# Kernel tuning notes

Measured on AMD Instinct MI355X. Metric: run time of the kernel, lower is better.

## Reference

```python
import jax, jax.numpy as jnp
import numpy as np
from jax import lax

NBITS = 8
QMAX_SYM = 2 ** (NBITS - 1) - 1  # 127
QMIN_SYM = -(2 ** (NBITS - 1))   # -128
QMAX_ASYM = 2 ** NBITS - 1       # 255


def fake_quant_sym(x):
    # symmetric per-tensor fake quant with straight-through estimator
    delta = lax.stop_gradient(jnp.max(jnp.abs(x))) / QMAX_SYM + 1e-8
    q = jnp.clip(jnp.round(x / delta), QMIN_SYM, QMAX_SYM) * delta
    return x + lax.stop_gradient(q - x)


def fake_quant_asym(x):
    # asymmetric per-tensor fake quant (for softmax output) with STE
    xmin = lax.stop_gradient(jnp.min(x))
    xmax = lax.stop_gradient(jnp.max(x))
    delta = (xmax - xmin) / QMAX_ASYM + 1e-8
    zp = jnp.round(-xmin / delta)
    q = (jnp.clip(jnp.round(x / delta) + zp, 0, QMAX_ASYM) - zp) * delta
    return x + lax.stop_gradient(q - x)


def layer_norm(x, g, b, eps=1e-5):
    mu = jnp.mean(x, axis=-1, keepdims=True)
    var = jnp.var(x, axis=-1, keepdims=True)
    return (x - mu) * lax.rsqrt(var + eps) * g + b


def setup_inputs() -> dict:
    key = jax.random.key(0)
    ks = jax.random.split(key, 8)
    B, N, C = 8, 4096, 256
    s = 0.02
    return {
        "x": jax.random.normal(ks[0], (B, N, C), jnp.float32),
        "q_w": jax.random.normal(ks[1], (C, C), jnp.float32) * s,
        "q_b": jnp.zeros((C,), jnp.float32),
        "kv_w": jax.random.normal(ks[2], (2 * C, C), jnp.float32) * s,
        "kv_b": jnp.zeros((2 * C,), jnp.float32),
        "sr_w": jax.random.normal(ks[3], (C, C, 4, 4), jnp.float32) * s,
        "sr_b": jnp.zeros((C,), jnp.float32),
        "norm_g": jnp.ones((C,), jnp.float32),
        "norm_b": jnp.zeros((C,), jnp.float32),
        "proj_w": jax.random.normal(ks[4], (C, C), jnp.float32) * s,
        "proj_b": jnp.zeros((C,), jnp.float32),
        "H": 64,
        "W": 64,
    }


def reference(x, q_w, q_b, kv_w, kv_b, sr_w, sr_b, norm_g, norm_b, proj_w, proj_b, H, W):
    B, N, C = x.shape
    num_heads = 8
    sr_ratio = 4
    dh = C // num_heads
    scale = dh ** -0.5

    # weight fake-quant (PreQuantModule, sym=True)
    q_wq = fake_quant_sym(q_w)
    kv_wq = fake_quant_sym(kv_w)
    sr_wq = fake_quant_sym(sr_w)
    proj_wq = fake_quant_sym(proj_w)

    # q projection -> [B, heads, N, dh], post-act sym fake quant
    q = (jnp.einsum('bnc,dc->bnd', x, q_wq) + q_b)
    q = fake_quant_sym(q.reshape(B, N, num_heads, dh).transpose(0, 2, 1, 3))

    # spatial reduction: x -> [B,C,H,W], conv k=stride=sr_ratio, then LayerNorm
    x_ = x.transpose(0, 2, 1).reshape(B, C, H, W)
    x_ = lax.conv_general_dilated(x_, sr_wq, (sr_ratio, sr_ratio), 'VALID',
                                  dimension_numbers=('NCHW', 'OIHW', 'NCHW'))
    x_ = x_ + sr_b[None, :, None, None]
    N2 = (H // sr_ratio) * (W // sr_ratio)
    x_ = x_.reshape(B, C, N2).transpose(0, 2, 1)  # [B, N2, C]
    x_ = layer_norm(x_, norm_g, norm_b)

    # kv projection -> k, v [B, heads, N2, dh], post-act sym fake quant
    kv = jnp.einsum('bnc,dc->bnd', x_, kv_wq) + kv_b
    kv = kv.reshape(B, N2, 2, num_heads, dh).transpose(2, 0, 3, 1, 4)
    k = fake_quant_sym(kv[0])
    v = fake_quant_sym(kv[1])

    # attention with asym fake quant on softmax output
    attn = jnp.einsum('bhnd,bhmd->bhnm', q, k) * scale
    attn = jax.nn.softmax(attn, axis=-1)
    attn = fake_quant_asym(attn)

    out = jnp.einsum('bhnm,bhmd->bhnd', attn, v)
    out = out.transpose(0, 2, 1, 3).reshape(B, N, C)
    out = jnp.einsum('bnc,dc->bnd', out, proj_wq) + proj_b
    return out
```

## Files before the change

### kernel.cpp

```cpp
#include <hip/hip_runtime.h>
#include <stdint.h>

typedef float f32x4 __attribute__((ext_vector_type(4)));
typedef __bf16 bf16x8 __attribute__((ext_vector_type(8)));

#define DEV __device__ __forceinline__

DEV unsigned short f2bf(float f) {
  unsigned u = __float_as_uint(f);
  u += 0x7FFFu + ((u >> 16) & 1u);
  return (unsigned short)(u >> 16);
}

DEV float exp2_(float x) {
#if __has_builtin(__builtin_amdgcn_exp2f)
  return __builtin_amdgcn_exp2f(x);
#else
  return exp2f(x);
#endif
}

DEV unsigned cvtpk(float lo, float hi) {
  unsigned r;
  asm("v_cvt_pk_bf16_f32 %0, %1, %2" : "=v"(r) : "v"(lo), "v"(hi));
  return r;
}

DEV void pl32swap(unsigned &a, unsigned &b) {
#if __has_builtin(__builtin_amdgcn_permlane32_swap)
  auto r = __builtin_amdgcn_permlane32_swap(a, b, false, false);
  a = r[0]; b = r[1];
#else
  asm("v_permlane32_swap_b32 %0, %1" : "+v"(a), "+v"(b));
#endif
}

DEV void pl16swap(unsigned &a, unsigned &b) {
#if __has_builtin(__builtin_amdgcn_permlane16_swap)
  auto r = __builtin_amdgcn_permlane16_swap(a, b, false, false);
  a = r[0]; b = r[1];
#else
  asm("v_permlane16_swap_b32 %0, %1" : "+v"(a), "+v"(b));
#endif
}

DEV uint4 qfrag4(uint4 w, float idq, float dq) {
  unsigned o[4];
  const unsigned* wi = &w.x;
  #pragma unroll
  for (int i = 0; i < 4; i++) {
    float lo = __uint_as_float(wi[i] << 16);
    float hi = __uint_as_float(wi[i] & 0xffff0000u);
    lo = fminf(fmaxf(rintf(lo * idq), -128.f), 127.f) * dq;
    hi = fminf(fmaxf(rintf(hi * idq), -128.f), 127.f) * dq;
    o[i] = cvtpk(lo, hi);
  }
  return make_uint4(o[0], o[1], o[2], o[3]);
}

DEV bf16x8 qfrag(uint4 w, float idq, float dq) {
  uint4 r = qfrag4(w, idq, dq);
  return *(bf16x8*)&r;
}

__global__ void k_init(float* scal) {
  int t = threadIdx.x;
  if (t < 16) scal[t] = (t == 7) ? __uint_as_float(0x7f800000u) : 0.f;
}

__global__ __launch_bounds__(256) void k_absmax4(const float* w0, const float* w1,
                                                 const float* w2, const float* w3, float* scal) {
  const float* srcs[4] = {w0, w1, w2, w3};
  const int ns[4] = {65536, 131072, 1048576, 65536};
  int t = blockIdx.y;
  const float* src = srcs[t];
  int n = ns[t];
  float m = 0.f;
  for (int i = blockIdx.x * 256 + threadIdx.x; i < n; i += gridDim.x * 256)
    m = fmaxf(m, fabsf(src[i]));
  #pragma unroll
  for (int d = 1; d < 64; d <<= 1) m = fmaxf(m, __shfl_xor(m, d, 64));
  __shared__ float red[4];
  if ((threadIdx.x & 63) == 0) red[threadIdx.x >> 6] = m;
  __syncthreads();
  if (threadIdx.x == 0) {
    m = fmaxf(fmaxf(red[0], red[1]), fmaxf(red[2], red[3]));
    atomicMax((unsigned*)(scal + t), __float_as_uint(m));
  }
}

__global__ __launch_bounds__(256) void k_quantw(const float* qw, const float* kvw,
                                                const float* prw, const float* srw,
                                                const float* xf,
                                                unsigned short* qo, unsigned short* kvo,
                                                unsigned short* pro, unsigned short* sro,
                                                unsigned short* xbo,
                                                const float* scal) {
  int bx = blockIdx.x;
  int tid = bx * 256 + threadIdx.x;
  {
    int oo = tid >> 12;
    int rem = tid & 4095;
    int khkw = rem >> 8;
    int i = rem & 255;
    float delta = scal[2] / 127.f + 1e-8f;
    float x = srw[oo * 4096 + i * 16 + khkw];
    sro[tid] = f2bf(fminf(fmaxf(rintf(x / delta), -128.f), 127.f) * delta);
  }
  {
    const float4* xs = (const float4*)(xf + (size_t)tid * 8);
    float4 v0 = xs[0], v1 = xs[1];
    unsigned w0 = ((unsigned)f2bf(v0.y) << 16) | f2bf(v0.x);
    unsigned w1 = ((unsigned)f2bf(v0.w) << 16) | f2bf(v0.z);
    unsigned w2 = ((unsigned)f2bf(v1.y) << 16) | f2bf(v1.x);
    unsigned w3 = ((unsigned)f2bf(v1.w) << 16) | f2bf(v1.z);
    *(uint4*)(xbo + (size_t)tid * 8) = make_uint4(w0, w1, w2, w3);
  }
  if (bx < 512) {
    float delta = scal[1] / 127.f + 1e-8f;
    kvo[tid] = f2bf(fminf(fmaxf(rintf(kvw[tid] / delta), -128.f), 127.f) * delta);
  }
  if (bx < 256) {
    float dq = scal[0] / 127.f + 1e-8f;
    qo[tid] = f2bf(fminf(fmaxf(rintf(qw[tid] / dq), -128.f), 127.f) * dq);
    float dp = scal[3] / 127.f + 1e-8f;
    pro[tid] = f2bf(fminf(fmaxf(rintf(prw[tid] / dp), -128.f), 127.f) * dp);
  }
}

__global__ __launch_bounds__(256) void k_gemm_qkv(const unsigned short* __restrict__ xnrm,
                                                  const unsigned short* __restrict__ kvw,
                                                  const float* __restrict__ kvb,
                                                  const unsigned short* __restrict__ xb,
                                                  const unsigned short* __restrict__ qw,
                                                  const float* __restrict__ qb,
                                                  unsigned short* __restrict__ kqu,
                                                  unsigned short* __restrict__ vqtu,
                                                  unsigned short* __restrict__ qq,
                                                  float* scal) {
  __shared__ unsigned short smem[18432];
  const int tid = threadIdx.x;
  const int wid = tid >> 6, lane = tid & 63;
  const int quad = lane >> 4, lr = lane & 15;
  const int wm = wid >> 1, wn = wid & 1;
  if (blockIdx.x < 256) {
    unsigned short* As = smem;
    unsigned short* Bs = smem + 8704;
    const int n0 = (blockIdx.x & 7) * 64, m0 = (blockIdx.x >> 3) * 64;
    f32x4 acc[2][2] = {};
    for (int kb = 0; kb < 256; kb += 128) {
      __syncthreads();
      #pragma unroll
      for (int i = 0; i < 4; i++) {
        int c = i * 256 + tid;
        int row = c >> 4, cu = (c & 15) * 8;
        *(uint4*)&As[row * 136 + cu] = *(const uint4*)(xnrm + (size_t)(m0 + row) * 256 + kb + cu);
        *(uint4*)&Bs[row * 136 + cu] = *(const uint4*)(kvw + (size_t)(n0 + row) * 256 + kb + cu);
      }
      __syncthreads();
      #pragma unroll
      for (int kc = 0; kc < 4; kc++) {
        bf16x8 af0 = *(const bf16x8*)&As[(wm * 32 + lr) * 136 + kc * 32 + quad * 8];
        bf16x8 af1 = *(const bf16x8*)&As[(wm * 32 + 16 + lr) * 136 + kc * 32 + quad * 8];
        bf16x8 bf0 = *(const bf16x8*)&Bs[(wn * 32 + lr) * 136 + kc * 32 + quad * 8];
        bf16x8 bf1 = *(const bf16x8*)&Bs[(wn * 32 + 16 + lr) * 136 + kc * 32 + quad * 8];
        acc[0][0] = __builtin_amdgcn_mfma_f32_16x16x32_bf16(af0, bf0, acc[0][0], 0, 0, 0);
        acc[0][1] = __builtin_amdgcn_mfma_f32_16x16x32_bf16(af0, bf1, acc[0][1], 0, 0, 0);
        acc[1][0] = __builtin_amdgcn_mfma_f32_16x16x32_bf16(af1, bf0, acc[1][0], 0, 0, 0);
        acc[1][1] = __builtin_amdgcn_mfma_f32_16x16x32_bf16(af1, bf1, acc[1][1], 0, 0, 0);
      }
    }
    float amax = 0.f;
    #pragma unroll
    for (int mi = 0; mi < 2; mi++)
      #pragma unroll
      for (int ni = 0; ni < 2; ni++) {
        int col = n0 + wn * 32 + ni * 16 + lr;
        float bv = kvb[col];
        #pragma unroll
        for (int r = 0; r < 4; r++) {
          int row = m0 + wm * 32 + mi * 16 + quad * 4 + r;
          float v = acc[mi][ni][r] + bv;
          int b = row >> 8, n2 = row & 255;
          int h = (col >> 5) & 7, j = col & 31;
          if (col < 256)
            kqu[((size_t)((b * 8 + h) * 256 + n2)) * 32 + j] = f2bf(v);
          else
            vqtu[((size_t)((b * 8 + h) * 32 + j)) * 256 + n2] = f2bf(v);
          amax = fmaxf(amax, fabsf(v));
        }
      }
    #pragma unroll
    for (int d = 1; d < 64; d <<= 1) amax = fmaxf(amax, __shfl_xor(amax, d, 64));
    if (lane == 0)
      atomicMax((unsigned*)(scal + 5 + (n0 >= 256 ? 1 : 0)), __float_as_uint(amax));
  } else {
    unsigned short* As = smem;
    unsigned short* Bs = smem + 9216;
    const int id = blockIdx.x - 256;
    const int xcd = id & 7, idx = id >> 3;
    const int mt = xcd * 32 + (idx >> 1), nt = idx & 1;
    const int m0 = mt * 128, n0 = nt * 128;
    f32x4 acc[4][4] = {};
    for (int kb = 0; kb < 256; kb += 64) {
      __syncthreads();
      #pragma unroll
      for (int i = 0; i < 4; i++) {
        int c = i * 256 + tid;
        int row = c >> 3, cu = (c & 7) * 8;
        *(uint4*)&As[row * 72 + cu] = *(const uint4*)(xb + (size_t)(m0 + row) * 256 + kb + cu);
        *(uint4*)&Bs[row * 72 + cu] = *(const uint4*)(qw + (size_t)(n0 + row) * 256 + kb + cu);
      }
      __syncthreads();
      #pragma unroll
      for (int kc = 0; kc < 2; kc++) {
        bf16x8 af[4], bf[4];
        #pragma unroll
        for (int mi = 0; mi < 4; mi++)
          af[mi] = *(const bf16x8*)&As[(wm * 64 + mi * 16 + lr) * 72 + kc * 32 + quad * 8];
        #pragma unroll
        for (int ni = 0; ni < 4; ni++)
          bf[ni] = *(const bf16x8*)&Bs[(wn * 64 + ni * 16 + lr) * 72 + kc * 32 + quad * 8];
        #pragma unroll
        for (int mi = 0; mi < 4; mi++)
          #pragma unroll
          for (int ni = 0; ni < 4; ni++)
            acc[mi][ni] = __builtin_amdgcn_mfma_f32_16x16x32_bf16(af[mi], bf[ni], acc[mi][ni], 0, 0, 0);
      }
    }
    float amax = 0.f;
    #pragma unroll
    for (int mi = 0; mi < 4; mi++)
      #pragma unroll
      for (int ni = 0; ni < 4; ni++) {
        int col = n0 + wn * 64 + ni * 16 + lr;
        float bv = qb[col];
        #pragma unroll
        for (int r = 0; r < 4; r++) {
          int row = m0 + wm * 64 + mi * 16 + quad * 4 + r;
          float v = acc[mi][ni][r] + bv;
          int b = row >> 12, nn = row & 4095;
          int h = col >> 5, j = col & 31;
          qq[((size_t)(b * 8 + h) * 4096 + nn) * 32 + j] = f2bf(v);
          amax = fmaxf(amax, fabsf(v));
        }
      }
    #pragma unroll
    for (int d = 1; d < 64; d <<= 1) amax = fmaxf(amax, __shfl_xor(amax, d, 64));
    if (lane == 0) atomicMax((unsigned*)(scal + 4), __float_as_uint(amax));
  }
}

__global__ __launch_bounds__(256) void k_gemm128(const unsigned short* __restrict__ Ab,
                                                 const unsigned short* __restrict__ W,
                                                 const float* __restrict__ bias,
                                                 float* __restrict__ C) {
  __shared__ unsigned short As[128 * 72];
  __shared__ unsigned short Bs[128 * 72];
  const int id = blockIdx.x;
  const int xcd = id & 7, idx = id >> 3;
  const int mt = xcd * 32 + (idx >> 1), nt = idx & 1;
  const int m0 = mt * 128, n0 = nt * 128;
  const int tid = threadIdx.x;
  const int wid = tid >> 6, lane = tid & 63;
  const int quad = lane >> 4, lr = lane & 15;
  const int wm = wid >> 1, wn = wid & 1;
  f32x4 acc[4][4] = {};
  for (int kb = 0; kb < 256; kb += 64) {
    __syncthreads();
    #pragma unroll
    for (int i = 0; i < 4; i++) {
      int c = i * 256 + tid;
      int row = c >> 3, cu = (c & 7) * 8;
      *(uint4*)&As[row * 72 + cu] = *(const uint4*)(Ab + (size_t)(m0 + row) * 256 + kb + cu);
      *(uint4*)&Bs[row * 72 + cu] = *(const uint4*)(W + (size_t)(n0 + row) * 256 + kb + cu);
    }
    __syncthreads();
    #pragma unroll
    for (int kc = 0; kc < 2; kc++) {
      bf16x8 af[4], bf[4];
      #pragma unroll
      for (int mi = 0; mi < 4; mi++)
        af[mi] = *(const bf16x8*)&As[(wm * 64 + mi * 16 + lr) * 72 + kc * 32 + quad * 8];
      #pragma unroll
      for (int ni = 0; ni < 4; ni++)
        bf[ni] = *(const bf16x8*)&Bs[(wn * 64 + ni * 16 + lr) * 72 + kc * 32 + quad * 8];
      #pragma unroll
      for (int mi = 0; mi < 4; mi++)
        #pragma unroll
        for (int ni = 0; ni < 4; ni++)
          acc[mi][ni] = __builtin_amdgcn_mfma_f32_16x16x32_bf16(af[mi], bf[ni], acc[mi][ni], 0, 0, 0);
    }
  }
  #pragma unroll
  for (int mi = 0; mi < 4; mi++)
    #pragma unroll
    for (int ni = 0; ni < 4; ni++) {
      int col = n0 + wn * 64 + ni * 16 + lr;
      float bv = bias[col];
      #pragma unroll
      for (int r = 0; r < 4; r++) {
        int row = m0 + wm * 64 + mi * 16 + quad * 4 + r;
        C[(size_t)row * 256 + col] = acc[mi][ni][r] + bv;
      }
    }
}

__global__ __launch_bounds__(256) void k_conv_sk(const unsigned short* __restrict__ xb,
                                                 const unsigned short* __restrict__ W,
                                                 float* __restrict__ C) {
  __shared__ unsigned short As[64 * 136];
  __shared__ unsigned short Bs[64 * 136];
  const int id = blockIdx.x;
  const int xcd = id & 7, idx = id >> 3;
  const int a = idx >> 2, nt = idx & 3;
  const int ag = xcd * 16 + a;
  const int mt = ag & 31, z = ag >> 5;
  const int m0 = mt * 64, n0 = nt * 64;
  const int kOff = z * 1024;
  C += (size_t)z * 2048 * 256;
  const int tid = threadIdx.x;
  const int wid = tid >> 6, lane = tid & 63;
  const int quad = lane >> 4, lr = lane & 15;
  const int wm = wid >> 1, wn = wid & 1;
  f32x4 acc[2][2] = {};
  for (int kb = 0; kb < 1024; kb += 128) {
    __syncthreads();
    #pragma unroll
    for (int i = 0; i < 4; i++) {
      int c = i * 256 + tid;
      int row = c >> 4, cu = (c & 15) * 8;
      int kk = kOff + kb + cu;
      int m = m0 + row;
      int b = m >> 8, p = m & 255, ph = p >> 4, pw = p & 15;
      int q = kk >> 8, ii = kk & 255;
      int n = (ph * 4 + (q >> 2)) * 64 + pw * 4 + (q & 3);
      *(uint4*)&As[row * 136 + cu] = *(const uint4*)(xb + ((size_t)(b * 4096 + n) * 256 + ii));
      *(uint4*)&Bs[row * 136 + cu] = *(const uint4*)(W + (size_t)(n0 + row) * 4096 + kk);
    }
    __syncthreads();
    #pragma unroll
    for (int kc = 0; kc < 4; kc++) {
      bf16x8 af0 = *(const bf16x8*)&As[(wm * 32 + lr) * 136 + kc * 32 + quad * 8];
      bf16x8 af1 = *(const bf16x8*)&As[(wm * 32 + 16 + lr) * 136 + kc * 32 + quad * 8];
      bf16x8 bf0 = *(const bf16x8*)&Bs[(wn * 32 + lr) * 136 + kc * 32 + quad * 8];
      bf16x8 bf1 = *(const bf16x8*)&Bs[(wn * 32 + 16 + lr) * 136 + kc * 32 + quad * 8];
      acc[0][0] = __builtin_amdgcn_mfma_f32_16x16x32_bf16(af0, bf0, acc[0][0], 0, 0, 0);
      acc[0][1] = __builtin_amdgcn_mfma_f32_16x16x32_bf16(af0, bf1, acc[0][1], 0, 0, 0);
      acc[1][0] = __builtin_amdgcn_mfma_f32_16x16x32_bf16(af1, bf0, acc[1][0], 0, 0, 0);
      acc[1][1] = __builtin_amdgcn_mfma_f32_16x16x32_bf16(af1, bf1, acc[1][1], 0, 0, 0);
    }
  }
  #pragma unroll
  for (int mi = 0; mi < 2; mi++)
    #pragma unroll
    for (int ni = 0; ni < 2; ni++) {
      int col = n0 + wn * 32 + ni * 16 + lr;
      #pragma unroll
      for (int r = 0; r < 4; r++) {
        int row = m0 + wm * 32 + mi * 16 + quad * 4 + r;
        C[(size_t)row * 256 + col] = acc[mi][ni][r];
      }
    }
}

__global__ __launch_bounds__(256) void k_ln(const float* __restrict__ convp, const float* srb,
                                            const float* g, const float* bb,
                                            unsigned short* __restrict__ xn) {
  int row = blockIdx.x, c = threadIdx.x;
  float v = srb[c];
  #pragma unroll
  for (int s = 0; s < 4; s++) v += convp[s * 524288 + row * 256 + c];
  __shared__ float red[4];
  float s = v;
  #pragma unroll
  for (int d = 1; d < 64; d <<= 1) s += __shfl_xor(s, d, 64);
  if ((c & 63) == 0) red[c >> 6] = s;
  __syncthreads();
  float mu = (red[0] + red[1] + red[2] + red[3]) * (1.f / 256.f);
  __syncthreads();
  float dv = v - mu;
  float s2 = dv * dv;
  #pragma unroll
  for (int d = 1; d < 64; d <<= 1) s2 += __shfl_xor(s2, d, 64);
  if ((c & 63) == 0) red[c >> 6] = s2;
  __syncthreads();
  float var = (red[0] + red[1] + red[2] + red[3]) * (1.f / 256.f);
  float rs = 1.f / sqrtf(var + 1e-5f);
  xn[row * 256 + c] = f2bf(dv * rs * g[c] + bb[c]);
}

__global__ __launch_bounds__(256) void k_attn1(const unsigned short* __restrict__ qq,
                                               const unsigned short* __restrict__ kqu,
                                               float2* __restrict__ rowstats,
                                               float* scal) {
  __shared__ unsigned short KsL[8192];
  __shared__ float red[8];
  const int bh = blockIdx.y;
  const int row0 = blockIdx.x * 256;
  const int tid = threadIdx.x, wid = tid >> 6, lane = tid & 63, quad = lane >> 4, lr = lane & 15;
  const float c2 = 0.17677669529663687f * 1.4426950408889634f;
  const unsigned short* kb = kqu + (size_t)bh * 8192;
  float dk = scal[5] / 127.f + 1e-8f;
  float idk = 1.f / dk;
  float dq = scal[4] / 127.f + 1e-8f;
  float idq = 1.f / dq;
  #pragma unroll
  for (int k = 0; k < 4; k++) {
    int cid = k * 256 + tid;
    int seg = cid >> 6, lc = cid & 63, qc = lc >> 4, lrc = lc & 15;
    uint4 kw = *(const uint4*)(kb + (seg * 16 + lrc) * 32 + qc * 8);
    *(uint4*)&KsL[cid * 8] = qfrag4(kw, idk, dk);
  }
  __syncthreads();
  float wmin = 1e30f, wmax = 0.f;
  #pragma unroll
  for (int g = 0; g < 4; g++) {
    int rowg = row0 + g * 64 + wid * 16 + lr;
    uint4 qw = *(const uint4*)(qq + ((size_t)bh * 4096 + rowg) * 32 + quad * 8);
    bf16x8 qf = qfrag(qw, idq, dq);
    f32x4 acc[16] = {};
    #pragma unroll
    for (int t = 0; t < 16; t++) {
      bf16x8 kf = *(const bf16x8*)&KsL[(t * 64 + quad * 16 + lr) * 8];
      acc[t] = __builtin_amdgcn_mfma_f32_16x16x32_bf16(kf, qf, acc[t], 0, 0, 0);
    }
    float mxr = -1e30f, mnr = 1e30f;
    #pragma unroll
    for (int t = 0; t < 16; t++)
      #pragma unroll
      for (int r = 0; r < 4; r++) {
        float s = acc[t][r];
        mxr = fmaxf(mxr, s); mnr = fminf(mnr, s);
      }
    #pragma unroll
    for (int d = 16; d < 64; d <<= 1) {
      mxr = fmaxf(mxr, __shfl_xor(mxr, d, 64));
      mnr = fminf(mnr, __shfl_xor(mnr, d, 64));
    }
    float m2 = mxr * c2;
    float l = 0.f;
    #pragma unroll
    for (int t = 0; t < 16; t++)
      #pragma unroll
      for (int r = 0; r < 4; r++)
        l += exp2_(fmaf(acc[t][r], c2, -m2));
    #pragma unroll
    for (int d = 16; d < 64; d <<= 1) l += __shfl_xor(l, d, 64);
    float inv_l = 1.f / l;
    if (lane < 16)
      rowstats[(size_t)bh * 4096 + rowg] = make_float2(m2, inv_l);
    wmax = fmaxf(wmax, inv_l);
    wmin = fminf(wmin, exp2_((mnr - mxr) * c2) * inv_l);
  }
  #pragma unroll
  for (int d = 1; d < 16; d <<= 1) {
    wmax = fmaxf(wmax, __shfl_xor(wmax, d, 64));
    wmin = fminf(wmin, __shfl_xor(wmin, d, 64));
  }
  if (lane == 0) { red[wid] = wmin; red[4 + wid] = wmax; }
  __syncthreads();
  if (tid == 0) {
    float mn = fminf(fminf(red[0], red[1]), fminf(red[2], red[3]));
    float mx = fmaxf(fmaxf(red[4], red[5]), fmaxf(red[6], red[7]));
    atomicMin((unsigned*)(scal + 7), __float_as_uint(mn));
    atomicMax((unsigned*)(scal + 8), __float_as_uint(mx));
  }
}

__global__ __launch_bounds__(256) void k_attn2(const unsigned short* __restrict__ qq,
                                               const unsigned short* __restrict__ kqu,
                                               const unsigned short* __restrict__ vqtu,
                                               const float* scal,
                                               const float2* __restrict__ rowstats,
                                               unsigned short* __restrict__ attn_out) {
  __shared__ unsigned short KsL[8192];
  __shared__ unsigned short VsL[8192];
  const int bh = blockIdx.y, b = bh >> 3, h = bh & 7;
  const int row0 = blockIdx.x * 256;
  const int tid = threadIdx.x, wid = tid >> 6, lane = tid & 63, quad = lane >> 4, lr = lane & 15;
  const float c2 = 0.17677669529663687f * 1.4426950408889634f;
  const unsigned short* kb = kqu + (size_t)bh * 8192;
  const unsigned short* vb = vqtu + (size_t)bh * 8192;
  float dk = scal[5] / 127.f + 1e-8f;
  float idk = 1.f / dk;
  float dv = scal[6] / 127.f + 1e-8f;
  float idv = 1.f / dv;
  float dq = scal[4] / 127.f + 1e-8f;
  float idq = 1.f / dq;
  #pragma unroll
  for (int k = 0; k < 4; k++) {
    int cid = k * 256 + tid;
    int seg = cid >> 6, lc = cid & 63, qc = lc >> 4, lrc = lc & 15;
    uint4 kw = *(const uint4*)(kb + (seg * 16 + lrc) * 32 + qc * 8);
    *(uint4*)&KsL[cid * 8] = qfrag4(kw, idk, dk);
    uint4 vw = *(const uint4*)(vb + ((seg & 1) * 16 + lrc) * 256 + (seg >> 1) * 32 + qc * 8);
    *(uint4*)&VsL[cid * 8] = qfrag4(vw, idv, dv);
  }
  float pmin = scal[7], pmax = scal[8];
  float delta = (pmax - pmin) / 255.f + 1e-8f;
  float zp = rintf(-pmin / delta);
  float qlo = -zp, qhi = 255.f - zp;
  __syncthreads();
  #pragma unroll
  for (int g = 0; g < 4; g++) {
    int rowg = row0 + g * 64 + wid * 16 + lr;
    uint4 qw = *(const uint4*)(qq + ((size_t)bh * 4096 + rowg) * 32 + quad * 8);
    bf16x8 qf = qfrag(qw, idq, dq);
    float2 st = rowstats[(size_t)bh * 4096 + rowg];
    f32x4 acc[16] = {};
    #pragma unroll
    for (int t = 0; t < 16; t++) {
      bf16x8 kf = *(const bf16x8*)&KsL[(t * 64 + quad * 16 + lr) * 8];
      acc[t] = __builtin_amdgcn_mfma_f32_16x16x32_bf16(kf, qf, acc[t], 0, 0, 0);
    }
    float ofs = __log2f(st.y / delta) - st.x;
    f32x4 o0 = {}, o1 = {};
    #pragma unroll
    for (int ks = 0; ks < 8; ks++) {
      float pv[8];
      #pragma unroll
      for (int half = 0; half < 2; half++) {
        #pragma unroll
        for (int r = 0; r < 4; r++) {
          float v = exp2_(fmaf(acc[2 * ks + half][r], c2, ofs));
          pv[half * 4 + r] = fminf(fmaxf(rintf(v), qlo), qhi) * delta;
        }
      }
      unsigned wa = cvtpk(pv[0], pv[1]);
      unsigned wb = cvtpk(pv[2], pv[3]);
      unsigned wc = cvtpk(pv[4], pv[5]);
      unsigned wd = cvtpk(pv[6], pv[7]);
      pl32swap(wa, wc);
      pl16swap(wa, wc);
      pl32swap(wb, wd);
      pl16swap(wb, wd);
      uint4 w = make_uint4(wa, wb, wc, wd);
      bf16x8 pa = *(bf16x8*)&w;
      bf16x8 b0 = *(const bf16x8*)&VsL[((ks * 2 + 0) * 64 + quad * 16 + lr) * 8];
      bf16x8 b1 = *(const bf16x8*)&VsL[((ks * 2 + 1) * 64 + quad * 16 + lr) * 8];
      o0 = __builtin_amdgcn_mfma_f32_16x16x32_bf16(pa, b0, o0, 0, 0, 0);
      o1 = __builtin_amdgcn_mfma_f32_16x16x32_bf16(pa, b1, o1, 0, 0, 0);
    }
    #pragma unroll
    for (int r = 0; r < 4; r++) {
      int n = row0 + g * 64 + wid * 16 + quad * 4 + r;
      size_t base = ((size_t)(b * 4096) + n) * 256 + h * 32;
      attn_out[base + lr] = f2bf(o0[r]);
      attn_out[base + 16 + lr] = f2bf(o1[r]);
    }
  }
}

extern "C" void kernel_launch(void* const* d_in, const int* in_sizes, int n_in,
                              void* d_out, int out_size, void* d_ws, size_t ws_size,
                              hipStream_t stream) {
  const float* x      = (const float*)d_in[0];
  const float* q_w    = (const float*)d_in[1];
  const float* q_b    = (const float*)d_in[2];
  const float* kv_w   = (const float*)d_in[3];
  const float* kv_b   = (const float*)d_in[4];
  const float* sr_w   = (const float*)d_in[5];
  const float* sr_b   = (const float*)d_in[6];
  const float* norm_g = (const float*)d_in[7];
  const float* norm_b = (const float*)d_in[8];
  const float* proj_w = (const float*)d_in[9];
  const float* proj_b = (const float*)d_in[10];
  float* out = (float*)d_out;

  char* ws = (char*)d_ws;
  float* scal = (float*)ws;
  unsigned short* q_wq    = (unsigned short*)(ws + 256);
  unsigned short* kv_wq   = (unsigned short*)(ws + 131328);
  unsigned short* proj_wq = (unsigned short*)(ws + 393472);
  unsigned short* sr_wq   = (unsigned short*)(ws + 524544);
  unsigned short* xn      = (unsigned short*)(ws + 2621696);
  unsigned short* kqu     = (unsigned short*)(ws + 7864576);
  unsigned short* vqtu    = (unsigned short*)(ws + 8913152);
  float2*         rowstats= (float2*)(ws + 9961728);
  float*          convp   = (float*)(ws + 12058880);
  unsigned short* attn_o  = (unsigned short*)(ws + 12058880);
  unsigned short* qq      = (unsigned short*)(ws + 45613312);
  unsigned short* xb      = (unsigned short*)(ws + 62390528);

  k_init<<<1, 64, 0, stream>>>(scal);
  k_absmax4<<<dim3(64, 4), 256, 0, stream>>>(q_w, kv_w, sr_w, proj_w, scal);
  k_quantw<<<4096, 256, 0, stream>>>(q_w, kv_w, proj_w, sr_w, x,
                                     q_wq, kv_wq, proj_wq, sr_wq, xb, scal);
  k_conv_sk<<<512, 256, 0, stream>>>(xb, sr_wq, convp);
  k_ln<<<2048, 256, 0, stream>>>(convp, sr_b, norm_g, norm_b, xn);
  k_gemm_qkv<<<768, 256, 0, stream>>>(xn, kv_wq, kv_b, xb, q_wq, q_b,
                                      kqu, vqtu, qq, scal);
  k_attn1<<<dim3(16, 64), 256, 0, stream>>>(qq, kqu, rowstats, scal);
  k_attn2<<<dim3(16, 64), 256, 0, stream>>>(qq, kqu, vqtu, scal, rowstats, attn_o);
  k_gemm128<<<512, 256, 0, stream>>>(attn_o, proj_wq, proj_b, out);
}
```

Measured before the change: 272.3 us.

## Split attn1 into more blocks and replace global atomics with partial-stat reduction kernel

The attention statistics kernel now processes 128 rows per block instead of 256, which doubles the grid to 2048 blocks for better occupancy across CUs. Each block writes its min/max to a per-block partial array instead of doing global atomicMin/atomicMax. A new single-block kernel then reduces those partials into the scalar slots. This removes atomic contention and adds one extra small kernel launch plus a redundant K-tile load per extra block.

```diff
diff --git a/kernel.cpp b/kernel.cpp
--- a/kernel.cpp
+++ b/kernel.cpp
@@ -393,11 +393,12 @@
 __global__ __launch_bounds__(256) void k_attn1(const unsigned short* __restrict__ qq,
                                                const unsigned short* __restrict__ kqu,
                                                float2* __restrict__ rowstats,
-                                               float* scal) {
+                                               const float* __restrict__ scal,
+                                               float2* __restrict__ pstat) {
   __shared__ unsigned short KsL[8192];
   __shared__ float red[8];
   const int bh = blockIdx.y;
-  const int row0 = blockIdx.x * 256;
+  const int row0 = blockIdx.x * 128;
   const int tid = threadIdx.x, wid = tid >> 6, lane = tid & 63, quad = lane >> 4, lr = lane & 15;
   const float c2 = 0.17677669529663687f * 1.4426950408889634f;
   const unsigned short* kb = kqu + (size_t)bh * 8192;
@@ -415,7 +416,7 @@
   __syncthreads();
   float wmin = 1e30f, wmax = 0.f;
   #pragma unroll
-  for (int g = 0; g < 4; g++) {
+  for (int g = 0; g < 2; g++) {
     int rowg = row0 + g * 64 + wid * 16 + lr;
     uint4 qw = *(const uint4*)(qq + ((size_t)bh * 4096 + rowg) * 32 + quad * 8);
     bf16x8 qf = qfrag(qw, idq, dq);
@@ -463,15 +464,36 @@
   if (tid == 0) {
     float mn = fminf(fminf(red[0], red[1]), fminf(red[2], red[3]));
     float mx = fmaxf(fmaxf(red[4], red[5]), fmaxf(red[6], red[7]));
-    atomicMin((unsigned*)(scal + 7), __float_as_uint(mn));
-    atomicMax((unsigned*)(scal + 8), __float_as_uint(mx));
+    pstat[blockIdx.y * 32 + blockIdx.x] = make_float2(mn, mx);
+  }
+}
+
+__global__ __launch_bounds__(256) void k_pminmax(const float2* __restrict__ pstat, float* scal) {
+  int t = threadIdx.x;
+  float mn = 1e30f, mx = 0.f;
+  #pragma unroll
+  for (int i = 0; i < 8; i++) {
+    float2 v = pstat[t + i * 256];
+    mn = fminf(mn, v.x); mx = fmaxf(mx, v.y);
+  }
+  #pragma unroll
+  for (int d = 1; d < 64; d <<= 1) {
+    mn = fminf(mn, __shfl_xor(mn, d, 64));
+    mx = fmaxf(mx, __shfl_xor(mx, d, 64));
+  }
+  __shared__ float red[8];
+  if ((t & 63) == 0) { red[t >> 6] = mn; red[4 + (t >> 6)] = mx; }
+  __syncthreads();
+  if (t == 0) {
+    scal[7] = fminf(fminf(red[0], red[1]), fminf(red[2], red[3]));
+    scal[8] = fmaxf(fmaxf(red[4], red[5]), fmaxf(red[6], red[7]));
   }
 }
 
 __global__ __launch_bounds__(256) void k_attn2(const unsigned short* __restrict__ qq,
                                                const unsigned short* __restrict__ kqu,
                                                const unsigned short* __restrict__ vqtu,
-                                               const float* scal,
+                                               const float* __restrict__ scal,
                                                const float2* __restrict__ rowstats,
                                                unsigned short* __restrict__ attn_out) {
   __shared__ unsigned short KsL[8192];
@@ -580,6 +602,7 @@
   float2*         rowstats= (float2*)(ws + 9961728);
   float*          convp   = (float*)(ws + 12058880);
   unsigned short* attn_o  = (unsigned short*)(ws + 12058880);
+  float2*         pstat   = (float2*)(ws + 28836096);
   unsigned short* qq      = (unsigned short*)(ws + 45613312);
   unsigned short* xb      = (unsigned short*)(ws + 62390528);
 
@@ -591,7 +614,8 @@
   k_ln<<<2048, 256, 0, stream>>>(convp, sr_b, norm_g, norm_b, xn);
   k_gemm_qkv<<<768, 256, 0, stream>>>(xn, kv_wq, kv_b, xb, q_wq, q_b,
                                       kqu, vqtu, qq, scal);
-  k_attn1<<<dim3(16, 64), 256, 0, stream>>>(qq, kqu, rowstats, scal);
+  k_attn1<<<dim3(32, 64), 256, 0, stream>>>(qq, kqu, rowstats, scal, pstat);
+  k_pminmax<<<1, 256, 0, stream>>>(pstat, scal);
   k_attn2<<<dim3(16, 64), 256, 0, stream>>>(qq, kqu, vqtu, scal, rowstats, attn_o);
   k_gemm128<<<512, 256, 0, stream>>>(attn_o, proj_wq, proj_b, out);
 }
```

Result: faster. 259.4 us (-4.7%).
